# Optimization experiments

Hardware: AMD Instinct MI355X
Metric: run time of the kernel (lower is better)

## Reference

```python
import jax, jax.numpy as jnp
import numpy as np

NUM_STEPS = 96  # ray samples M; ProSTGrid's step count, fixed for static shapes


def _transform_mat3x4(pose):
    # pose: [B,6] -> rigid transform [B,3,4], matches set_matrix (Rz@Ry@Rx@T)
    B = pose.shape[0]
    rx, ry, rz, tx, ty, tz = [pose[:, i] for i in range(6)]
    o = jnp.zeros((B,), pose.dtype)
    l = jnp.ones((B,), pose.dtype)
    cx, sx = jnp.cos(rx), jnp.sin(rx)
    cy, sy = jnp.cos(ry), jnp.sin(ry)
    cz, sz = jnp.cos(rz), jnp.sin(rz)
    Rx = jnp.stack([jnp.stack([l, o, o, o], -1), jnp.stack([o, cx, -sx, o], -1),
                    jnp.stack([o, sx, cx, o], -1), jnp.stack([o, o, o, l], -1)], 1)
    Ry = jnp.stack([jnp.stack([cy, o, sy, o], -1), jnp.stack([o, l, o, o], -1),
                    jnp.stack([-sy, o, cy, o], -1), jnp.stack([o, o, o, l], -1)], 1)
    Rz = jnp.stack([jnp.stack([cz, -sz, o, o], -1), jnp.stack([sz, cz, o, o], -1),
                    jnp.stack([o, o, l, o], -1), jnp.stack([o, o, o, l], -1)], 1)
    T = jnp.stack([jnp.stack([l, o, o, tx], -1), jnp.stack([o, l, o, ty], -1),
                   jnp.stack([o, o, l, tz], -1), jnp.stack([o, o, o, l], -1)], 1)
    M = Rz @ Ry @ Rx @ T
    return M[:, :3, :]


def _raydist_range(T, corner_pt, src):
    # inv_pose_vec + raydist_range
    t = T[:, :3, 3]
    R = T[:, :3, :3]
    pt = corner_pt - t[:, None, :]
    inv_pt = pt @ jnp.linalg.inv(R)          # pt.bmm(inv(R))
    inv_pt = inv_pt.at[:, :, 2].set(src - inv_pt[:, :, 2])
    dist = jnp.sqrt(jnp.sum(inv_pt * inv_pt, axis=-1))
    return jnp.min(dist), jnp.max(dist)


def _make_grid(H, W, M, dmin, dmax, src, det, pix_spacing):
    # Cone-beam sampling grid: source at (0,0,src), detector plane z = src-det.
    ys = (jnp.arange(H, dtype=jnp.float32) - (H - 1) / 2.0) * pix_spacing
    xs = (jnp.arange(W, dtype=jnp.float32) - (W - 1) / 2.0) * pix_spacing
    yy, xx = jnp.meshgrid(ys, xs, indexing='ij')          # [H,W]
    dz = jnp.full_like(xx, -det)
    dirv = jnp.stack([xx, yy, dz], -1)                    # detector - source
    dirv = dirv / jnp.linalg.norm(dirv, axis=-1, keepdims=True)
    dists = jnp.linspace(dmin, dmax, M)                   # [M]
    src_pt = jnp.stack([jnp.zeros(()), jnp.zeros(()), src])
    pts = src_pt + dirv[:, :, None, :] * dists[None, None, :, None]  # [H,W,M,3]
    ones = jnp.ones(pts.shape[:-1] + (1,), pts.dtype)
    return jnp.concatenate([pts, ones], -1).reshape(1, H * W * M, 4)


def _trilinear_5d(vol, grid):
    # faithful port of _bilinear_interpolate_no_torch_5D (8-corner gather+blend)
    B, C, D, Hv, Wv = vol.shape
    im_flat = jnp.transpose(vol, (0, 2, 3, 4, 1)).reshape(-1, C)  # [B*D*H*W, C]
    _, oD, oH, oW, _ = grid.shape
    x = (Wv * (grid[..., 0] * 0.5 + 0.5)).reshape(-1)
    y = (Hv * (grid[..., 1] * 0.5 + 0.5)).reshape(-1)
    z = (D * (grid[..., 2] * 0.5 + 0.5)).reshape(-1)
    oob = ~((x >= 0) & (x <= Wv) & (y >= 0) & (y <= Hv) & (z >= 0) & (z <= D))
    x0 = jnp.clip(jnp.floor(x), 0, Wv - 1); x1 = jnp.clip(jnp.floor(x) + 1, 0, Wv - 1)
    y0 = jnp.clip(jnp.floor(y), 0, Hv - 1); y1 = jnp.clip(jnp.floor(y) + 1, 0, Hv - 1)
    z0 = jnp.clip(jnp.floor(z), 0, D - 1);  z1 = jnp.clip(jnp.floor(z) + 1, 0, D - 1)
    base = jnp.repeat(jnp.arange(B, dtype=jnp.int32) * (D * Hv * Wv), oD * oH * oW)
    def gather(zc, yc, xc):
        idx = base + zc.astype(jnp.int32) * (Hv * Wv) + yc.astype(jnp.int32) * Wv + xc.astype(jnp.int32)
        return im_flat[idx]
    Ia, Ib = gather(z0, y0, x0), gather(z0, y0, x1)
    Ic, Id = gather(z0, y1, x0), gather(z0, y1, x1)
    Ie, If = gather(z1, y0, x0), gather(z1, y0, x1)
    Ig, Ih = gather(z1, y1, x0), gather(z1, y1, x1)
    wa = ((x1 - x) * (y1 - y) * (z1 - z))[:, None]
    wb = ((x - x0) * (y1 - y) * (z1 - z))[:, None]
    wc = ((x1 - x) * (y - y0) * (z1 - z))[:, None]
    wd = ((x - x0) * (y - y0) * (z1 - z))[:, None]
    we = ((x1 - x) * (y1 - y) * (z - z0))[:, None]
    wf = ((x - x0) * (y1 - y) * (z - z0))[:, None]
    wg = ((x1 - x) * (y - y0) * (z - z0))[:, None]
    wh = ((x - x0) * (y - y0) * (z - z0))[:, None]
    acc = wa * Ia + wb * Ib + wc * Ic + wd * Id + we * Ie + wf * If + wg * Ig + wh * Ih
    acc = jnp.where(oob[:, None], 0.0, acc)
    out = acc.reshape(B, oD, oH, oW, C)
    return jnp.transpose(out, (0, 4, 1, 2, 3))


def setup_inputs() -> dict:
    key = jax.random.key(0)
    k1, k2, k3 = jax.random.split(key, 3)
    D, H, W = 128, 256, 256
    ct = jax.random.normal(k1, (1, 1, D, D, D), jnp.float32)
    fixed = jax.random.normal(k2, (1, 1, H, W), jnp.float32)
    pose = jax.random.normal(k3, (1, 6), jnp.float32) * 0.1
    corner_pt = jnp.array([[[sx, sy, sz] for sx in (-1.0, 1.0) for sy in (-1.0, 1.0)
                            for sz in (-1.0, 1.0)]], jnp.float32)  # [1,8,3]
    # param = (src, det, pix_spacing, step_size), volume normalized to [-1,1]^3
    param = jnp.array([4.0, 8.0, 4.0 / W, 0.02], jnp.float32)
    return {"ct": ct, "fixed": fixed, "pose": pose, "corner_pt": corner_pt,
            "param": param, "H": H, "W": W}


def reference(ct, fixed, pose, corner_pt, param, H, W):
    src, det, pix_spacing = param[0], param[1], param[2]
    T = _transform_mat3x4(pose)                                # [1,3,4]
    dmin, dmax = _raydist_range(T, corner_pt, src)
    dmin = jax.lax.stop_gradient(dmin)                         # .data in torch
    dmax = jax.lax.stop_gradient(dmax)
    grid = _make_grid(H, W, NUM_STEPS, dmin, dmax, src, det, pix_spacing)  # [1,HWM,4]
    grid_trans = (grid @ jnp.swapaxes(T, 1, 2)).reshape(1, H, W, NUM_STEPS, 3)
    x_3d = _trilinear_5d(ct, grid_trans)                       # [1,C,H,W,M]
    moving = jnp.sum(x_3d, axis=-1)                            # integrate along rays
    return moving
```

## Files before the change

kernel.cpp:

```cpp
#include <hip/hip_runtime.h>

#define NUM_STEPS 96
#define SPLIT 4
#define STEPS_PER_THREAD (NUM_STEPS / SPLIT)
#define VD 128
#define VSLICE (VD * VD)

__global__ __launch_bounds__(256) void prost_fwd_kernel(
    const float* __restrict__ ct,
    const float* __restrict__ pose,
    const float* __restrict__ corner,
    const float* __restrict__ param,
    const int* __restrict__ Hp,
    const int* __restrict__ Wp,
    float* __restrict__ out,
    int n)
{
    const int gid = blockIdx.x * blockDim.x + threadIdx.x;
    const int idx = gid >> 2;
    const int seg = gid & 3;
    if (idx >= n) return;

    const int H = *Hp;
    const int W = *Wp;
    const int h = idx / W;
    const int w = idx % W;

    const float rx = pose[0], ry = pose[1], rz = pose[2];
    const float tx = pose[3], ty = pose[4], tz = pose[5];
    const float cx = cosf(rx), sx = sinf(rx);
    const float cy = cosf(ry), sy = sinf(ry);
    const float cz = cosf(rz), sz = sinf(rz);

    const float r00 = cz * cy;
    const float r01 = -sz * cx + cz * sy * sx;
    const float r02 = sz * sx + cz * sy * cx;
    const float r10 = sz * cy;
    const float r11 = cz * cx + sz * sy * sx;
    const float r12 = -cz * sx + sz * sy * cx;
    const float r20 = -sy;
    const float r21 = cy * sx;
    const float r22 = cy * cx;

    const float t0 = r00 * tx + r01 * ty + r02 * tz;
    const float t1 = r10 * tx + r11 * ty + r12 * tz;
    const float t2 = r20 * tx + r21 * ty + r22 * tz;

    const float src = param[0];
    const float det = param[1];
    const float pix = param[2];

    float dmin = 1e30f, dmax = -1e30f;
    #pragma unroll
    for (int c = 0; c < 8; ++c) {
        const float px = corner[c * 3 + 0] - t0;
        const float py = corner[c * 3 + 1] - t1;
        const float pz = corner[c * 3 + 2] - t2;
        const float ix = r00 * px + r01 * py + r02 * pz;
        const float iy = r10 * px + r11 * py + r12 * pz;
        float iz = r20 * px + r21 * py + r22 * pz;
        iz = src - iz;
        const float d = sqrtf(ix * ix + iy * iy + iz * iz);
        dmin = fminf(dmin, d);
        dmax = fmaxf(dmax, d);
    }

    const float ys = ((float)h - (float)(H - 1) * 0.5f) * pix;
    const float xs = ((float)w - (float)(W - 1) * 0.5f) * pix;
    const float dz = -det;
    const float invn = 1.0f / sqrtf(xs * xs + ys * ys + dz * dz);
    const float nx = xs * invn;
    const float ny = ys * invn;
    const float nz = dz * invn;

    const float Ax = 64.0f * (r00 * nx + r01 * ny + r02 * nz);
    const float Bx = 64.0f * (r02 * src + t0) + 64.0f;
    const float Ay = 64.0f * (r10 * nx + r11 * ny + r12 * nz);
    const float By = 64.0f * (r12 * src + t1) + 64.0f;
    const float Az = 64.0f * (r20 * nx + r21 * ny + r22 * nz);
    const float Bz = 64.0f * (r22 * src + t2) + 64.0f;

    const float step = (dmax - dmin) / (float)(NUM_STEPS - 1);

    const int m0 = seg * STEPS_PER_THREAD;
    float acc = 0.0f;

    #pragma unroll 4
    for (int k = 0; k < STEPS_PER_THREAD; ++k) {
        const int m = m0 + k;
        const float d = dmin + step * (float)m;
        const float X = Ax * d + Bx;
        const float Y = Ay * d + By;
        const float Z = Az * d + Bz;

        const bool inb = (X >= 0.0f) & (X <= 128.0f) &
                         (Y >= 0.0f) & (Y <= 128.0f) &
                         (Z >= 0.0f) & (Z <= 128.0f);

        const float fx = floorf(X), fy = floorf(Y), fz = floorf(Z);
        const float x0 = fminf(fmaxf(fx,        0.0f), 127.0f);
        const float x1 = fminf(fmaxf(fx + 1.0f, 0.0f), 127.0f);
        const float y0 = fminf(fmaxf(fy,        0.0f), 127.0f);
        const float y1 = fminf(fmaxf(fy + 1.0f, 0.0f), 127.0f);
        const float z0 = fminf(fmaxf(fz,        0.0f), 127.0f);
        const float z1 = fminf(fmaxf(fz + 1.0f, 0.0f), 127.0f);

        const float wx1 = X - x0, wx0 = x1 - X;
        const float wy1 = Y - y0, wy0 = y1 - Y;
        const float wz1 = Z - z0, wz0 = z1 - Z;

        const int ix0 = (int)x0, ix1 = (int)x1;
        const int iy0 = (int)y0, iy1 = (int)y1;
        const int iz0 = (int)z0, iz1 = (int)z1;

        const float* p00 = ct + iz0 * VSLICE + iy0 * VD;
        const float* p01 = ct + iz0 * VSLICE + iy1 * VD;
        const float* p10 = ct + iz1 * VSLICE + iy0 * VD;
        const float* p11 = ct + iz1 * VSLICE + iy1 * VD;

        const float Ia = p00[ix0], Ib = p00[ix1];
        const float Ic = p01[ix0], Id = p01[ix1];
        const float Ie = p10[ix0], If = p10[ix1];
        const float Ig = p11[ix0], Ih = p11[ix1];

        const float s =
            wz0 * (wy0 * (wx0 * Ia + wx1 * Ib) + wy1 * (wx0 * Ic + wx1 * Id)) +
            wz1 * (wy0 * (wx0 * Ie + wx1 * If) + wy1 * (wx0 * Ig + wx1 * Ih));
        acc += inb ? s : 0.0f;
    }

    acc += __shfl_xor(acc, 1);
    acc += __shfl_xor(acc, 2);

    if (seg == 0) out[idx] = acc;
}

extern "C" void kernel_launch(void* const* d_in, const int* in_sizes, int n_in,
                              void* d_out, int out_size, void* d_ws, size_t ws_size,
                              hipStream_t stream) {
    const float* ct     = (const float*)d_in[0];
    const float* pose   = (const float*)d_in[2];
    const float* corner = (const float*)d_in[3];
    const float* param  = (const float*)d_in[4];
    const int*   Hp     = (const int*)d_in[5];
    const int*   Wp     = (const int*)d_in[6];
    float* out = (float*)d_out;

    const int n = out_size;
    const int total = n * SPLIT;
    const int block = 256;
    const int grid = (total + block - 1) / block;
    prost_fwd_kernel<<<grid, block, 0, stream>>>(ct, pose, corner, param, Hp, Wp, out, n);
}
```

Baseline: 37.00 us.

## Repack CT volume into float4 x/z-neighbor texels to halve gather loads

Adds a pre-pass that builds a workspace volume of float4 entries holding each voxel plus its x+1, z+1 and x+1/z+1 neighbours. The trilinear sampler then issues two 16-byte loads per sample instead of eight scalar gathers. Out-of-bounds samples are masked through the z weights rather than a final select. The cost is an extra kernel launch each call that reads 8 MB and writes a 32 MB repacked volume, with a fallback to the old kernel when the workspace is too small.

```diff
diff --git a/kernel.cpp b/kernel.cpp
--- a/kernel.cpp
+++ b/kernel.cpp
@@ -2,30 +2,35 @@
 
 #define NUM_STEPS 96
 #define SPLIT 4
-#define STEPS_PER_THREAD (NUM_STEPS / SPLIT)
+#define SPT (NUM_STEPS / SPLIT)
 #define VD 128
 #define VSLICE (VD * VD)
-
-__global__ __launch_bounds__(256) void prost_fwd_kernel(
-    const float* __restrict__ ct,
-    const float* __restrict__ pose,
-    const float* __restrict__ corner,
-    const float* __restrict__ param,
-    const int* __restrict__ Hp,
-    const int* __restrict__ Wp,
-    float* __restrict__ out,
-    int n)
-{
-    const int gid = blockIdx.x * blockDim.x + threadIdx.x;
-    const int idx = gid >> 2;
-    const int seg = gid & 3;
-    if (idx >= n) return;
-
-    const int H = *Hp;
-    const int W = *Wp;
-    const int h = idx / W;
-    const int w = idx % W;
-
+#define NVOX (VD * VD * VD)
+#define VOL4_BYTES ((size_t)NVOX * 16)
+
+__global__ __launch_bounds__(256) void prost_repack_kernel(
+    const float* __restrict__ ct, float4* __restrict__ vol4)
+{
+    const int i = blockIdx.x * 256 + threadIdx.x;
+    const int x = i & (VD - 1);
+    const int y = (i >> 7) & (VD - 1);
+    const int z = i >> 14;
+    const int xp = min(x + 1, VD - 1);
+    const int zp = min(z + 1, VD - 1);
+    const float* r0 = ct + (z  << 14) + (y << 7);
+    const float* r1 = ct + (zp << 14) + (y << 7);
+    float4 q;
+    q.x = r0[x]; q.y = r0[xp];
+    q.z = r1[x]; q.w = r1[xp];
+    vol4[i] = q;
+}
+
+__device__ __forceinline__ void prost_setup(
+    const float* __restrict__ pose, const float* __restrict__ corner,
+    const float* __restrict__ param, int h, int w, int H, int W,
+    float& Ax, float& Bx, float& Ay, float& By, float& Az, float& Bz,
+    float& dmin, float& step)
+{
     const float rx = pose[0], ry = pose[1], rz = pose[2];
     const float tx = pose[3], ty = pose[4], tz = pose[5];
     const float cx = cosf(rx), sx = sinf(rx);
@@ -50,7 +55,8 @@
     const float det = param[1];
     const float pix = param[2];
 
-    float dmin = 1e30f, dmax = -1e30f;
+    float dmax = -1e30f;
+    dmin = 1e30f;
     #pragma unroll
     for (int c = 0; c < 8; ++c) {
         const float px = corner[c * 3 + 0] - t0;
@@ -73,22 +79,45 @@
     const float ny = ys * invn;
     const float nz = dz * invn;
 
-    const float Ax = 64.0f * (r00 * nx + r01 * ny + r02 * nz);
-    const float Bx = 64.0f * (r02 * src + t0) + 64.0f;
-    const float Ay = 64.0f * (r10 * nx + r11 * ny + r12 * nz);
-    const float By = 64.0f * (r12 * src + t1) + 64.0f;
-    const float Az = 64.0f * (r20 * nx + r21 * ny + r22 * nz);
-    const float Bz = 64.0f * (r22 * src + t2) + 64.0f;
-
-    const float step = (dmax - dmin) / (float)(NUM_STEPS - 1);
-
-    const int m0 = seg * STEPS_PER_THREAD;
+    Ax = 64.0f * (r00 * nx + r01 * ny + r02 * nz);
+    Bx = 64.0f * (r02 * src + t0) + 64.0f;
+    Ay = 64.0f * (r10 * nx + r11 * ny + r12 * nz);
+    By = 64.0f * (r12 * src + t1) + 64.0f;
+    Az = 64.0f * (r20 * nx + r21 * ny + r22 * nz);
+    Bz = 64.0f * (r22 * src + t2) + 64.0f;
+
+    step = (dmax - dmin) / (float)(NUM_STEPS - 1);
+}
+
+__global__ __launch_bounds__(256) void prost_fwd_v4_kernel(
+    const float4* __restrict__ vol4,
+    const float* __restrict__ pose,
+    const float* __restrict__ corner,
+    const float* __restrict__ param,
+    const int* __restrict__ Hp,
+    const int* __restrict__ Wp,
+    float* __restrict__ out,
+    int n)
+{
+    const int gid = blockIdx.x * blockDim.x + threadIdx.x;
+    const int idx = gid >> 2;
+    const int seg = gid & 3;
+    if (idx >= n) return;
+
+    const int H = *Hp;
+    const int W = *Wp;
+    const int h = idx / W;
+    const int w = idx % W;
+
+    float Ax, Bx, Ay, By, Az, Bz, dmin, step;
+    prost_setup(pose, corner, param, h, w, H, W, Ax, Bx, Ay, By, Az, Bz, dmin, step);
+
+    const int m0 = seg * SPT;
     float acc = 0.0f;
 
-    #pragma unroll 4
-    for (int k = 0; k < STEPS_PER_THREAD; ++k) {
-        const int m = m0 + k;
-        const float d = dmin + step * (float)m;
+    #pragma unroll 6
+    for (int k = 0; k < SPT; ++k) {
+        const float d = dmin + step * (float)(m0 + k);
         const float X = Ax * d + Bx;
         const float Y = Ay * d + By;
         const float Z = Az * d + Bz;
@@ -107,16 +136,88 @@
 
         const float wx1 = X - x0, wx0 = x1 - X;
         const float wy1 = Y - y0, wy0 = y1 - Y;
-        const float wz1 = Z - z0, wz0 = z1 - Z;
+        const float wz0 = inb ? (z1 - Z) : 0.0f;
+        const float wz1 = inb ? (Z - z0) : 0.0f;
+
+        const int ix0 = (int)x0;
+        const int iy0 = (int)y0, iy1 = (int)y1;
+        const int iz0 = (int)z0;
+
+        const int rowa = (iz0 << 14) + (iy0 << 7) + ix0;
+        const int rowb = (iz0 << 14) + (iy1 << 7) + ix0;
+
+        const float4 qa = vol4[rowa];
+        const float4 qb = vol4[rowb];
+
+        acc += wz0 * (wy0 * (wx0 * qa.x + wx1 * qa.y) +
+                      wy1 * (wx0 * qb.x + wx1 * qb.y)) +
+               wz1 * (wy0 * (wx0 * qa.z + wx1 * qa.w) +
+                      wy1 * (wx0 * qb.z + wx1 * qb.w));
+    }
+
+    acc += __shfl_xor(acc, 1);
+    acc += __shfl_xor(acc, 2);
+
+    if (seg == 0) out[idx] = acc;
+}
+
+__global__ __launch_bounds__(256) void prost_fwd_kernel(
+    const float* __restrict__ ct,
+    const float* __restrict__ pose,
+    const float* __restrict__ corner,
+    const float* __restrict__ param,
+    const int* __restrict__ Hp,
+    const int* __restrict__ Wp,
+    float* __restrict__ out,
+    int n)
+{
+    const int gid = blockIdx.x * blockDim.x + threadIdx.x;
+    const int idx = gid >> 2;
+    const int seg = gid & 3;
+    if (idx >= n) return;
+
+    const int H = *Hp;
+    const int W = *Wp;
+    const int h = idx / W;
+    const int w = idx % W;
+
+    float Ax, Bx, Ay, By, Az, Bz, dmin, step;
+    prost_setup(pose, corner, param, h, w, H, W, Ax, Bx, Ay, By, Az, Bz, dmin, step);
+
+    const int m0 = seg * SPT;
+    float acc = 0.0f;
+
+    #pragma unroll 4
+    for (int k = 0; k < SPT; ++k) {
+        const float d = dmin + step * (float)(m0 + k);
+        const float X = Ax * d + Bx;
+        const float Y = Ay * d + By;
+        const float Z = Az * d + Bz;
+
+        const bool inb = (X >= 0.0f) & (X <= 128.0f) &
+                         (Y >= 0.0f) & (Y <= 128.0f) &
+                         (Z >= 0.0f) & (Z <= 128.0f);
+
+        const float fx = floorf(X), fy = floorf(Y), fz = floorf(Z);
+        const float x0 = fminf(fmaxf(fx,        0.0f), 127.0f);
+        const float x1 = fminf(fmaxf(fx + 1.0f, 0.0f), 127.0f);
+        const float y0 = fminf(fmaxf(fy,        0.0f), 127.0f);
+        const float y1 = fminf(fmaxf(fy + 1.0f, 0.0f), 127.0f);
+        const float z0 = fminf(fmaxf(fz,        0.0f), 127.0f);
+        const float z1 = fminf(fmaxf(fz + 1.0f, 0.0f), 127.0f);
+
+        const float wx1 = X - x0, wx0 = x1 - X;
+        const float wy1 = Y - y0, wy0 = y1 - Y;
+        const float wz0 = z1 - Z, wz1 = Z - z0;
 
         const int ix0 = (int)x0, ix1 = (int)x1;
         const int iy0 = (int)y0, iy1 = (int)y1;
         const int iz0 = (int)z0, iz1 = (int)z1;
 
-        const float* p00 = ct + iz0 * VSLICE + iy0 * VD;
-        const float* p01 = ct + iz0 * VSLICE + iy1 * VD;
-        const float* p10 = ct + iz1 * VSLICE + iy0 * VD;
-        const float* p11 = ct + iz1 * VSLICE + iy1 * VD;
+        const float* p00 = ct + (iz0 << 14) + (iy0 << 7);
+        const float* p01 = ct + (iz0 << 14) + (iy1 << 7);
+        const float* p10 = ct + (iz1 << 14) + (iy0 << 7);
+        const float* p11 = ct + (iz1 << 14) + (iy1 << 7);
 
         const float Ia = p00[ix0], Ib = p00[ix1];
         const float Ic = p01[ix0], Id = p01[ix1];
@@ -150,5 +251,14 @@
     const int total = n * SPLIT;
     const int block = 256;
     const int grid = (total + block - 1) / block;
-    prost_fwd_kernel<<<grid, block, 0, stream>>>(ct, pose, corner, param, Hp, Wp, out, n);
-}
+
+    if (ws_size >= VOL4_BYTES) {
+        float4* vol4 = (float4*)d_ws;
+        prost_repack_kernel<<<NVOX / 256, 256, 0, stream>>>(ct, vol4);
+        prost_fwd_v4_kernel<<<grid, block, 0, stream>>>(vol4, pose, corner, param,
+                                                        Hp, Wp, out, n);
+    } else {
+        prost_fwd_kernel<<<grid, block, 0, stream>>>(ct, pose, corner, param,
+                                                     Hp, Wp, out, n);
+    }
+}
```

Result: slower. 39.15 us (+5.8%).

## Split each ray's samples across two blocks and combine with atomics

Applied to the files above, without the earlier changes.

Each ray's 96 samples are now split into 8 segments over two blocks instead of 4 segments in one. Partial sums are combined with atomicAdd into an output zeroed by a memset. The goal is more parallelism and shorter per-thread loops, at the cost of twice the per-thread setup (pose trig, corner range), an extra memset launch, and atomic traffic. The launch bounds also now request 8 blocks per SM.

```diff
diff --git a/kernel.cpp b/kernel.cpp
--- a/kernel.cpp
+++ b/kernel.cpp
@@ -2,11 +2,12 @@
 
 #define NUM_STEPS 96
 #define SPLIT 4
-#define STEPS_PER_THREAD (NUM_STEPS / SPLIT)
+#define HALVES 2
+#define SPT (NUM_STEPS / (SPLIT * HALVES))
+#define PIX_PER_BLOCK 64
 #define VD 128
-#define VSLICE (VD * VD)
 
-__global__ __launch_bounds__(256) void prost_fwd_kernel(
+__global__ __launch_bounds__(256, 8) void prost_fwd_kernel(
     const float* __restrict__ ct,
     const float* __restrict__ pose,
     const float* __restrict__ corner,
@@ -16,9 +17,11 @@
     float* __restrict__ out,
     int n)
 {
-    const int gid = blockIdx.x * blockDim.x + threadIdx.x;
-    const int idx = gid >> 2;
-    const int seg = gid & 3;
+    const int tid  = threadIdx.x;
+    const int bid  = blockIdx.x;
+    const int half = bid & 1;
+    const int idx  = (bid >> 1) * PIX_PER_BLOCK + (tid >> 2);
+    const int seg  = tid & 3;
     if (idx >= n) return;
 
     const int H = *Hp;
@@ -82,13 +85,12 @@
 
     const float step = (dmax - dmin) / (float)(NUM_STEPS - 1);
 
-    const int m0 = seg * STEPS_PER_THREAD;
+    const int m0 = (half * SPLIT + seg) * SPT;
     float acc = 0.0f;
 
     #pragma unroll 4
-    for (int k = 0; k < STEPS_PER_THREAD; ++k) {
-        const int m = m0 + k;
-        const float d = dmin + step * (float)m;
+    for (int k = 0; k < SPT; ++k) {
+        const float d = dmin + step * (float)(m0 + k);
         const float X = Ax * d + Bx;
         const float Y = Ay * d + By;
         const float Z = Az * d + Bz;
@@ -107,16 +109,16 @@
 
         const float wx1 = X - x0, wx0 = x1 - X;
         const float wy1 = Y - y0, wy0 = y1 - Y;
-        const float wz1 = Z - z0, wz0 = z1 - Z;
+        const float wz0 = z1 - Z, wz1 = Z - z0;
 
         const int ix0 = (int)x0, ix1 = (int)x1;
         const int iy0 = (int)y0, iy1 = (int)y1;
         const int iz0 = (int)z0, iz1 = (int)z1;
 
-        const float* p00 = ct + iz0 * VSLICE + iy0 * VD;
-        const float* p01 = ct + iz0 * VSLICE + iy1 * VD;
-        const float* p10 = ct + iz1 * VSLICE + iy0 * VD;
-        const float* p11 = ct + iz1 * VSLICE + iy1 * VD;
+        const float* p00 = ct + (iz0 << 14) + (iy0 << 7);
+        const float* p01 = ct + (iz0 << 14) + (iy1 << 7);
+        const float* p10 = ct + (iz1 << 14) + (iy0 << 7);
+        const float* p11 = ct + (iz1 << 14) + (iy1 << 7);
 
         const float Ia = p00[ix0], Ib = p00[ix1];
         const float Ic = p01[ix0], Id = p01[ix1];
@@ -132,7 +134,7 @@
     acc += __shfl_xor(acc, 1);
     acc += __shfl_xor(acc, 2);
 
-    if (seg == 0) out[idx] = acc;
+    if (seg == 0) atomicAdd(&out[idx], acc);
 }
 
 extern "C" void kernel_launch(void* const* d_in, const int* in_sizes, int n_in,
@@ -147,8 +149,9 @@
     float* out = (float*)d_out;
 
     const int n = out_size;
-    const int total = n * SPLIT;
-    const int block = 256;
-    const int grid = (total + block - 1) / block;
-    prost_fwd_kernel<<<grid, block, 0, stream>>>(ct, pose, corner, param, Hp, Wp, out, n);
+    hipMemsetAsync(out, 0, (size_t)n * sizeof(float), stream);
+
+    const int blocks = ((n + PIX_PER_BLOCK - 1) / PIX_PER_BLOCK) * HALVES;
+    prost_fwd_kernel<<<blocks, 256, 0, stream>>>(ct, pose, corner, param,
+                                                 Hp, Wp, out, n);
 }
```

Measured after the change: 43.16 us. +16.7%, slower.

## Software-pipeline trilinear gathers in groups and remap block IDs across XCDs

Applied to the files above, without the earlier changes.

The per-thread sample loop is restructured into groups of three samples with double-buffered register arrays. Each group's eight gathers are issued before the previous group is blended, and sched_barrier stops the compiler from merging the two phases, so several loads stay in flight. Block IDs are also permuted so that neighbouring rays land on the same XCD for better L2 locality, and launch bounds now request three blocks per CU. The costs are higher register pressure and a possible loss of occupancy.

```diff
diff --git a/kernel.cpp b/kernel.cpp
--- a/kernel.cpp
+++ b/kernel.cpp
@@ -2,11 +2,12 @@
 
 #define NUM_STEPS 96
 #define SPLIT 4
-#define STEPS_PER_THREAD (NUM_STEPS / SPLIT)
+#define SPT (NUM_STEPS / SPLIT)
+#define GRP 3
+#define NGRP (SPT / GRP)
 #define VD 128
-#define VSLICE (VD * VD)
 
-__global__ __launch_bounds__(256) void prost_fwd_kernel(
+__global__ __launch_bounds__(256, 3) void prost_fwd_kernel(
     const float* __restrict__ ct,
     const float* __restrict__ pose,
     const float* __restrict__ corner,
@@ -16,7 +17,13 @@
     float* __restrict__ out,
     int n)
 {
-    const int gid = blockIdx.x * blockDim.x + threadIdx.x;
+    int bid = blockIdx.x;
+    const int nblk = gridDim.x;
+    if ((nblk & 7) == 0) {
+        bid = (bid & 7) * (nblk >> 3) + (bid >> 3);
+    }
+
+    const int gid = bid * 256 + threadIdx.x;
     const int idx = gid >> 2;
     const int seg = gid & 3;
     if (idx >= n) return;
@@ -81,52 +88,77 @@
     const float Bz = 64.0f * (r22 * src + t2) + 64.0f;
 
     const float step = (dmax - dmin) / (float)(NUM_STEPS - 1);
+    const int m0 = seg * SPT;
 
-    const int m0 = seg * STEPS_PER_THREAD;
+    float vA[GRP][8], wA[GRP][6];
+    float vB[GRP][8], wB[GRP][6];
+
+    auto stage = [&](int mbase, float (&v)[GRP][8], float (&wt)[GRP][6]) {
+        #pragma unroll
+        for (int j = 0; j < GRP; ++j) {
+            const float d = dmin + step * (float)(mbase + j);
+            const float X = Ax * d + Bx;
+            const float Y = Ay * d + By;
+            const float Z = Az * d + Bz;
+
+            const bool inb = (X >= 0.0f) & (X <= 128.0f) &
+                             (Y >= 0.0f) & (Y <= 128.0f) &
+                             (Z >= 0.0f) & (Z <= 128.0f);
+
+            const float fx = floorf(X), fy = floorf(Y), fz = floorf(Z);
+            const float x0 = fminf(fmaxf(fx,        0.0f), 127.0f);
+            const float x1 = fminf(fmaxf(fx + 1.0f, 0.0f), 127.0f);
+            const float y0 = fminf(fmaxf(fy,        0.0f), 127.0f);
+            const float y1 = fminf(fmaxf(fy + 1.0f, 0.0f), 127.0f);
+            const float z0 = fminf(fmaxf(fz,        0.0f), 127.0f);
+            const float z1 = fminf(fmaxf(fz + 1.0f, 0.0f), 127.0f);
+
+            wt[j][0] = x1 - X;
+            wt[j][1] = X - x0;
+            wt[j][2] = y1 - Y;
+            wt[j][3] = Y - y0;
+            wt[j][4] = inb ? (z1 - Z) : 0.0f;
+            wt[j][5] = inb ? (Z - z0) : 0.0f;
+
+            const int ix0 = (int)x0, ix1 = (int)x1;
+            const int zy00 = ((int)z0 << 14) + ((int)y0 << 7);
+            const int zy01 = ((int)z0 << 14) + ((int)y1 << 7);
+            const int zy10 = ((int)z1 << 14) + ((int)y0 << 7);
+            const int zy11 = ((int)z1 << 14) + ((int)y1 << 7);
+
+            v[j][0] = ct[zy00 + ix0];  v[j][1] = ct[zy00 + ix1];
+            v[j][2] = ct[zy01 + ix0];  v[j][3] = ct[zy01 + ix1];
+            v[j][4] = ct[zy10 + ix0];  v[j][5] = ct[zy10 + ix1];
+            v[j][6] = ct[zy11 + ix0];  v[j][7] = ct[zy11 + ix1];
+        }
+    };
+
     float acc = 0.0f;
+    auto blend = [&](const float (&v)[GRP][8], const float (&wt)[GRP][6]) {
+        #pragma unroll
+        for (int j = 0; j < GRP; ++j) {
+            const float wx0 = wt[j][0], wx1 = wt[j][1];
+            const float wy0 = wt[j][2], wy1 = wt[j][3];
+            const float wz0 = wt[j][4], wz1 = wt[j][5];
+            acc += wz0 * (wy0 * (wx0 * v[j][0] + wx1 * v[j][1]) +
+                          wy1 * (wx0 * v[j][2] + wx1 * v[j][3])) +
+                   wz1 * (wy0 * (wx0 * v[j][4] + wx1 * v[j][5]) +
+                          wy1 * (wx0 * v[j][6] + wx1 * v[j][7]));
+        }
+    };
 
-    #pragma unroll 4
-    for (int k = 0; k < STEPS_PER_THREAD; ++k) {
-        const int m = m0 + k;
-        const float d = dmin + step * (float)m;
-        const float X = Ax * d + Bx;
-        const float Y = Ay * d + By;
-        const float Z = Az * d + Bz;
-
-        const bool inb = (X >= 0.0f) & (X <= 128.0f) &
-                         (Y >= 0.0f) & (Y <= 128.0f) &
-                         (Z >= 0.0f) & (Z <= 128.0f);
-
-        const float fx = floorf(X), fy = floorf(Y), fz = floorf(Z);
-        const float x0 = fminf(fmaxf(fx,        0.0f), 127.0f);
-        const float x1 = fminf(fmaxf(fx + 1.0f, 0.0f), 127.0f);
-        const float y0 = fminf(fmaxf(fy,        0.0f), 127.0f);
-        const float y1 = fminf(fmaxf(fy + 1.0f, 0.0f), 127.0f);
-        const float z0 = fminf(fmaxf(fz,        0.0f), 127.0f);
-        const float z1 = fminf(fmaxf(fz + 1.0f, 0.0f), 127.0f);
-
-        const float wx1 = X - x0, wx0 = x1 - X;
-        const float wy1 = Y - y0, wy0 = y1 - Y;
-        const float wz1 = Z - z0, wz0 = z1 - Z;
-
-        const int ix0 = (int)x0, ix1 = (int)x1;
-        const int iy0 = (int)y0, iy1 = (int)y1;
-        const int iz0 = (int)z0, iz1 = (int)z1;
-
-        const float* p00 = ct + iz0 * VSLICE + iy0 * VD;
-        const float* p01 = ct + iz0 * VSLICE + iy1 * VD;
-        const float* p10 = ct + iz1 * VSLICE + iy0 * VD;
-        const float* p11 = ct + iz1 * VSLICE + iy1 * VD;
-
-        const float Ia = p00[ix0], Ib = p00[ix1];
-        const float Ic = p01[ix0], Id = p01[ix1];
-        const float Ie = p10[ix0], If = p10[ix1];
-        const float Ig = p11[ix0], Ih = p11[ix1];
-
-        const float s =
-            wz0 * (wy0 * (wx0 * Ia + wx1 * Ib) + wy1 * (wx0 * Ic + wx1 * Id)) +
-            wz1 * (wy0 * (wx0 * Ie + wx1 * If) + wy1 * (wx0 * Ig + wx1 * Ih));
-        acc += inb ? s : 0.0f;
+    stage(m0, vA, wA);
+    #pragma unroll
+    for (int g = 0; g < NGRP; ++g) {
+        if ((g & 1) == 0) {
+            if (g + 1 < NGRP) stage(m0 + (g + 1) * GRP, vB, wB);
+            __builtin_amdgcn_sched_barrier(0);
+            blend(vA, wA);
+        } else {
+            if (g + 1 < NGRP) stage(m0 + (g + 1) * GRP, vA, wA);
+            __builtin_amdgcn_sched_barrier(0);
+            blend(vB, wB);
+        }
     }
 
     acc += __shfl_xor(acc, 1);
@@ -150,5 +182,6 @@
     const int total = n * SPLIT;
     const int block = 256;
     const int grid = (total + block - 1) / block;
-    prost_fwd_kernel<<<grid, block, 0, stream>>>(ct, pose, corner, param, Hp, Wp, out, n);
+    prost_fwd_kernel<<<grid, block, 0, stream>>>(ct, pose, corner, param,
+                                                 Hp, Wp, out, n);
 }
```

New measurement: 90.25 us. 2.44x slower.
